# Kernel tuning notes

Hardware: AMD Instinct MI355X
Metric: run time of the kernel (lower is better)

The kernel has to match this reference:

```python
import jax, jax.numpy as jnp
import numpy as np
import math

B, T, D, H = 1, 2048, 1024, 16
DH = D // H  # 64


def relative_shift(x):
    # x: [B, H, T, S] -> Transformer-XL relative shift via zero-pad + reshape
    b, h, t, s = x.shape
    zero_pad = jnp.zeros((b, h, t, 1), dtype=x.dtype)
    x_padded = jnp.concatenate([zero_pad, x], axis=-1)       # [B,H,T,S+1]
    x_padded = x_padded.reshape(b, h, s + 1, t)              # [B,H,S+1,T]
    return x_padded[:, :, 1:].reshape(b, h, t, s)            # [B,H,T,S]


def setup_inputs() -> dict:
    key = jax.random.key(0)
    ks = jax.random.split(key, 9)
    std = 0.02
    return {
        "x": jax.random.normal(ks[0], (B, T, D), dtype=jnp.float32),
        "r_emb": jax.random.normal(ks[1], (T, D), dtype=jnp.float32),
        "Wq": jax.random.normal(ks[2], (D, D), dtype=jnp.float32) * std,
        "Wk": jax.random.normal(ks[3], (D, D), dtype=jnp.float32) * std,
        "Wv": jax.random.normal(ks[4], (D, D), dtype=jnp.float32) * std,
        "Wr": jax.random.normal(ks[5], (D, D), dtype=jnp.float32) * std,
        "Wo": jax.random.normal(ks[6], (D, D), dtype=jnp.float32) * std,
        "u": jax.random.normal(ks[7], (H, DH), dtype=jnp.float32) * std,
        "v_bias": jax.random.normal(ks[8], (H, DH), dtype=jnp.float32) * std,
    }


def reference(x, r_emb, Wq, Wk, Wv, Wr, Wo, u, v_bias):
    # mem=None path (the only shape-consistent path in the source), so S == T.
    b, t, d = x.shape
    s = t
    q = (x @ Wq).reshape(b, t, H, DH).transpose(0, 2, 1, 3)   # [B,H,T,DH]
    k = (x @ Wk).reshape(b, s, H, DH).transpose(0, 2, 1, 3)   # [B,H,S,DH]
    v = (x @ Wv).reshape(b, s, H, DH).transpose(0, 2, 1, 3)   # [B,H,S,DH]
    r = (r_emb @ Wr).reshape(r_emb.shape[0], H, DH)[-s:]       # [S,H,DH]

    AC = jnp.einsum('bhid,bhjd->bhij', q + u[None, :, None, :], k)
    BD = jnp.einsum('bhid,jhd->bhij', q + v_bias[None, :, None, :], r)
    BD = relative_shift(BD)

    attn = (AC + BD) / math.sqrt(DH)                           # [B,H,T,S]
    mask = jnp.tril(jnp.ones((t, s), dtype=bool))              # causal (S==T)
    attn = jnp.where(mask[None, None], attn, -jnp.inf)
    attn = jax.nn.softmax(attn, axis=-1)
    # dropout is identity in eval mode
    out = jnp.einsum('bhij,bhjd->bhid', attn, v)               # [B,H,T,DH]
    out = out.transpose(0, 2, 1, 3).reshape(b, t, d)           # [B,T,D]
    return out @ Wo
```

## Files before the change

### kernel.cpp

```cpp
#include <hip/hip_runtime.h>

typedef __bf16 bf16_t;
typedef __bf16 bf16x4v __attribute__((ext_vector_type(4)));
typedef __bf16 bf16x8 __attribute__((ext_vector_type(8)));
typedef float f32x4 __attribute__((ext_vector_type(4)));

constexpr int TT = 2048;
constexpr int DDIM = 1024;

constexpr size_t SZ_TD  = (size_t)2048 * 1024;
constexpr size_t OFF_QU = 0;
constexpr size_t OFF_QV = 1 * SZ_TD;
constexpr size_t OFF_KK = 2 * SZ_TD;
constexpr size_t OFF_RR = 3 * SZ_TD;
constexpr size_t OFF_VT = 4 * SZ_TD;
constexpr size_t OFF_AO = 5 * SZ_TD;
constexpr size_t OFF_XB = 6 * SZ_TD;
constexpr size_t OFF_RB = 7 * SZ_TD;
constexpr size_t OFF_WT = 8 * SZ_TD;
constexpr size_t SZ_W   = (size_t)1024 * 1024;

__device__ __forceinline__ f32x4 fzero4() {
  f32x4 z; z[0] = 0.f; z[1] = 0.f; z[2] = 0.f; z[3] = 0.f; return z;
}

__device__ __forceinline__ void gload16(const bf16_t* g, bf16_t* l) {
  __builtin_amdgcn_global_load_lds((const __attribute__((address_space(1))) void*)g,
                                   (__attribute__((address_space(3))) void*)l, 16, 0, 0);
}

__global__ __launch_bounds__(256) void convert_kernel(const float* __restrict__ x,
                                                      const float* __restrict__ r,
                                                      bf16_t* __restrict__ ws) {
  const int i = blockIdx.x * 256 + threadIdx.x;
  float4 a = ((const float4*)x)[i];
  float4 b = ((const float4*)r)[i];
  bf16x4v av, bv;
  av[0] = (bf16_t)a.x; av[1] = (bf16_t)a.y; av[2] = (bf16_t)a.z; av[3] = (bf16_t)a.w;
  bv[0] = (bf16_t)b.x; bv[1] = (bf16_t)b.y; bv[2] = (bf16_t)b.z; bv[3] = (bf16_t)b.w;
  ((bf16x4v*)(ws + OFF_XB))[i] = av;
  ((bf16x4v*)(ws + OFF_RB))[i] = bv;
}

__global__ __launch_bounds__(256) void transpose_w_kernel(const float* __restrict__ Wq,
                                                          const float* __restrict__ Wk,
                                                          const float* __restrict__ Wv,
                                                          const float* __restrict__ Wr,
                                                          const float* __restrict__ Wo,
                                                          bf16_t* __restrict__ ws) {
  const int k0 = blockIdx.x * 64, n0 = blockIdx.y * 64, wsel = blockIdx.z;
  const float* W = (wsel == 0) ? Wq : (wsel == 1) ? Wk : (wsel == 2) ? Wv : (wsel == 3) ? Wr : Wo;
  bf16_t* Wt = ws + OFF_WT + (size_t)wsel * SZ_W;
  __shared__ float tile[64][65];
  const int tid = threadIdx.x;
#pragma unroll
  for (int it = 0; it < 4; ++it) {
    int g = tid + it * 256; int rr = g >> 4; int c4 = (g & 15) * 4;
    float4 v = *(const float4*)&W[(size_t)(k0 + rr) * DDIM + n0 + c4];
    tile[rr][c4] = v.x; tile[rr][c4 + 1] = v.y; tile[rr][c4 + 2] = v.z; tile[rr][c4 + 3] = v.w;
  }
  __syncthreads();
#pragma unroll
  for (int it = 0; it < 4; ++it) {
    int g = tid + it * 256; int nr = g >> 4; int c4 = (g & 15) * 4;
    bf16x4v o;
    o[0] = (bf16_t)tile[c4 + 0][nr]; o[1] = (bf16_t)tile[c4 + 1][nr];
    o[2] = (bf16_t)tile[c4 + 2][nr]; o[3] = (bf16_t)tile[c4 + 3][nr];
    *(bf16x4v*)&Wt[(size_t)(n0 + nr) * DDIM + k0 + c4] = o;
  }
}

__device__ __forceinline__ void gemm128_core(const bf16_t* __restrict__ A,
                                             const bf16_t* __restrict__ Bt,
                                             int i0, int n0, int kbeg, int kend,
                                             f32x4 acc[4][4],
                                             bf16_t* As, bf16_t* Bs) {
  const int tid = threadIdx.x, lane = tid & 63, wv = tid >> 6;
  const int wr = (wv >> 1) * 64, wc = (wv & 1) * 64;
  const int sr = tid >> 2, scc = (tid & 3) * 8;
  const int l15 = lane & 15, lg8 = (lane >> 4) * 8;
  for (int k0 = kbeg; k0 < kend; k0 += 32) {
    __syncthreads();
    gload16(&A[(size_t)(i0 + sr) * DDIM + k0 + scc],       &As[sr * 32 + scc]);
    gload16(&A[(size_t)(i0 + 64 + sr) * DDIM + k0 + scc],  &As[(64 + sr) * 32 + scc]);
    gload16(&Bt[(size_t)(n0 + sr) * DDIM + k0 + scc],      &Bs[sr * 32 + scc]);
    gload16(&Bt[(size_t)(n0 + 64 + sr) * DDIM + k0 + scc], &Bs[(64 + sr) * 32 + scc]);
    __syncthreads();
    bf16x8 af[4], bfv[4];
#pragma unroll
    for (int m = 0; m < 4; ++m) af[m] = *(const bf16x8*)&As[(wr + m * 16 + l15) * 32 + lg8];
#pragma unroll
    for (int n = 0; n < 4; ++n) bfv[n] = *(const bf16x8*)&Bs[(wc + n * 16 + l15) * 32 + lg8];
#pragma unroll
    for (int m = 0; m < 4; ++m)
#pragma unroll
      for (int n = 0; n < 4; ++n)
        acc[m][n] = __builtin_amdgcn_mfma_f32_16x16x32_bf16(af[m], bfv[n], acc[m][n], 0, 0, 0);
  }
}

__global__ __launch_bounds__(256) void proj_kernel(const bf16_t* wsc, bf16_t* wsd,
                                                   const float* __restrict__ u,
                                                   const float* __restrict__ vb) {
  const int z = blockIdx.z;
  const int i0 = blockIdx.x * 128, n0 = blockIdx.y * 64;
  const bf16_t* A = wsc + ((z == 3) ? OFF_RB : OFF_XB);
  const bf16_t* Bt = wsc + OFF_WT + (size_t)z * SZ_W;
  __shared__ bf16_t As[128 * 32];
  __shared__ bf16_t Bs[64 * 32];
  const int tid = threadIdx.x, lane = tid & 63, wv = tid >> 6;
  const int wr = (wv >> 1) * 64, wc = (wv & 1) * 32;
  const int sr = tid >> 2, scc = (tid & 3) * 8;
  const int l15 = lane & 15, lg8 = (lane >> 4) * 8, lr4 = (lane >> 4) * 4;
  f32x4 acc[4][2];
#pragma unroll
  for (int m = 0; m < 4; ++m)
#pragma unroll
    for (int n = 0; n < 2; ++n) acc[m][n] = fzero4();

  for (int k0 = 0; k0 < DDIM; k0 += 32) {
    __syncthreads();
    gload16(&A[(size_t)(i0 + sr) * DDIM + k0 + scc],      &As[sr * 32 + scc]);
    gload16(&A[(size_t)(i0 + 64 + sr) * DDIM + k0 + scc], &As[(64 + sr) * 32 + scc]);
    gload16(&Bt[(size_t)(n0 + sr) * DDIM + k0 + scc],     &Bs[sr * 32 + scc]);
    __syncthreads();
    bf16x8 af[4], bfv[2];
#pragma unroll
    for (int m = 0; m < 4; ++m) af[m] = *(const bf16x8*)&As[(wr + m * 16 + l15) * 32 + lg8];
#pragma unroll
    for (int n = 0; n < 2; ++n) bfv[n] = *(const bf16x8*)&Bs[(wc + n * 16 + l15) * 32 + lg8];
#pragma unroll
    for (int m = 0; m < 4; ++m)
#pragma unroll
      for (int n = 0; n < 2; ++n)
        acc[m][n] = __builtin_amdgcn_mfma_f32_16x16x32_bf16(af[m], bfv[n], acc[m][n], 0, 0, 0);
  }

#pragma unroll
  for (int mm = 0; mm < 4; ++mm)
#pragma unroll
    for (int nn = 0; nn < 2; ++nn)
#pragma unroll
      for (int rg = 0; rg < 4; ++rg) {
        const int row = i0 + wr + mm * 16 + lr4 + rg;
        const int col = n0 + wc + nn * 16 + l15;
        const float val = acc[mm][nn][rg];
        const int hh = col >> 6, dh = col & 63;
        if (z == 0) {
          wsd[OFF_QU + ((size_t)hh * TT + row) * 64 + dh] = (bf16_t)(val + u[col]);
          wsd[OFF_QV + ((size_t)hh * TT + row) * 64 + dh] = (bf16_t)(val + vb[col]);
        } else if (z == 1) {
          wsd[OFF_KK + ((size_t)hh * TT + row) * 64 + dh] = (bf16_t)val;
        } else if (z == 2) {
          wsd[OFF_VT + ((size_t)hh * 64 + dh) * TT + row] = (bf16_t)val;
        } else {
          wsd[OFF_RR + ((size_t)hh * TT + (TT - 1 - row)) * 64 + dh] = (bf16_t)val;
        }
      }
}

#define SOFTPV(AC, PBX, PLX, QBASE, OO, MRUN, LRUN)                                        \
  {                                                                                        \
    float sc[4][4];                                                                        \
    float smax = -3e38f;                                                                   \
    _Pragma("unroll") for (int nt = 0; nt < 4; ++nt)                                       \
      _Pragma("unroll") for (int rg = 0; rg < 4; ++rg) {                                   \
        const int jj = nt * 16 + lg * 4 + rg;                                              \
        float v = (AC[nt][rg] + PBX[(l15 + 63 - jj) * 18 + l15]) * 0.125f;                 \
        v = (j0 + jj > (QBASE) + l15) ? -1e30f : v;                                        \
        smax = fmaxf(smax, v);                                                             \
        sc[nt][rg] = v;                                                                    \
      }                                                                                    \
    smax = fmaxf(smax, __shfl_xor(smax, 16));                                              \
    smax = fmaxf(smax, __shfl_xor(smax, 32));                                              \
    const float newm = fmaxf(MRUN, smax);                                                  \
    const float fac = __expf(MRUN - newm);                                                 \
    MRUN = newm;                                                                           \
    float pv[4][4];                                                                        \
    float rsum = 0.f;                                                                      \
    _Pragma("unroll") for (int nt = 0; nt < 4; ++nt)                                       \
      _Pragma("unroll") for (int rg = 0; rg < 4; ++rg) {                                   \
        pv[nt][rg] = __expf(sc[nt][rg] - newm);                                            \
        rsum += pv[nt][rg];                                                                \
      }                                                                                    \
    rsum += __shfl_xor(rsum, 16);                                                          \
    rsum += __shfl_xor(rsum, 32);                                                          \
    LRUN = LRUN * fac + rsum;                                                              \
    float fo[4];                                                                           \
    _Pragma("unroll") for (int rg = 0; rg < 4; ++rg) fo[rg] = __shfl(fac, lg * 4 + rg);    \
    _Pragma("unroll") for (int d = 0; d < 4; ++d)                                          \
      _Pragma("unroll") for (int rg = 0; rg < 4; ++rg) OO[d][rg] *= fo[rg];                \
    _Pragma("unroll") for (int nt = 0; nt < 4; ++nt) {                                     \
      bf16x4v pk;                                                                          \
      pk[0] = (bf16_t)pv[nt][0]; pk[1] = (bf16_t)pv[nt][1];                                \
      pk[2] = (bf16_t)pv[nt][2]; pk[3] = (bf16_t)pv[nt][3];                                \
      *(bf16x4v*)&PLX[l15 * 72 + nt * 16 + lg * 4] = pk;                                   \
    }                                                                                      \
    bf16x8 pf[2];                                                                          \
    _Pragma("unroll") for (int ks = 0; ks < 2; ++ks)                                       \
      pf[ks] = *(const bf16x8*)&PLX[l15 * 72 + ks * 32 + lg8];                             \
    _Pragma("unroll") for (int d = 0; d < 4; ++d)                                          \
      _Pragma("unroll") for (int ks = 0; ks < 2; ++ks)                                     \
        OO[d] = __builtin_amdgcn_mfma_f32_16x16x32_bf16(pf[ks], vf[d][ks], OO[d], 0, 0, 0);\
  }

__global__ __launch_bounds__(64) void attn_kernel(const bf16_t* wsc, bf16_t* wsd) {
  const int h = blockIdx.x;
  const int chunk = blockIdx.z;
  const int q32 = 63 - blockIdx.y;
  const int i0 = q32 * 32;
  const int lane = threadIdx.x & 63;
  const int l15 = lane & 15;
  const int lg = lane >> 4;
  const int lg8 = lg * 8;

  const int NT = (i0 >> 6) + 1;
  const int H = (NT + 1) >> 1;
  const int tbeg = chunk ? H : 0;
  const int tend = chunk ? NT : H;

  bf16_t* Po = wsd + ((chunk == 0) ? OFF_XB : OFF_RB) + (size_t)h * TT * 64;
  float2* ml = (float2*)(wsd + OFF_WT) + (size_t)(chunk * 16 + h) * TT;

  if (tbeg >= tend) {
#pragma unroll
    for (int m = 0; m < 2; ++m)
#pragma unroll
      for (int d = 0; d < 4; ++d)
#pragma unroll
        for (int rg = 0; rg < 4; ++rg)
          Po[(size_t)(i0 + m * 16 + lg * 4 + rg) * 64 + d * 16 + l15] = (bf16_t)0.f;
    if (lg == 0) { ml[i0 + l15] = make_float2(-3e38f, 0.f); ml[i0 + 16 + l15] = make_float2(-3e38f, 0.f); }
    return;
  }

  const bf16_t* QUp = wsc + OFF_QU + (size_t)h * TT * 64;
  const bf16_t* QVp = wsc + OFF_QV + (size_t)h * TT * 64;
  const bf16_t* Kp  = wsc + OFF_KK + (size_t)h * TT * 64;
  const bf16_t* Rp  = wsc + OFF_RR + (size_t)h * TT * 64;
  const bf16_t* Vp  = wsc + OFF_VT + (size_t)h * 64 * TT;

  __shared__ float PB1[80 * 18];
  __shared__ float PB2[80 * 18];
  __shared__ bf16_t PL1[16 * 72];
  __shared__ bf16_t PL2[16 * 72];

  bf16x8 qu1[2], qv1[2], qu2[2], qv2[2];
#pragma unroll
  for (int ks = 0; ks < 2; ++ks) {
    qu1[ks] = *(const bf16x8*)&QUp[(size_t)(i0 + l15) * 64 + ks * 32 + lg8];
    qv1[ks] = *(const bf16x8*)&QVp[(size_t)(i0 + l15) * 64 + ks * 32 + lg8];
    qu2[ks] = *(const bf16x8*)&QUp[(size_t)(i0 + 16 + l15) * 64 + ks * 32 + lg8];
    qv2[ks] = *(const bf16x8*)&QVp[(size_t)(i0 + 16 + l15) * 64 + ks * 32 + lg8];
  }

  f32x4 o1[4], o2[4];
#pragma unroll
  for (int d = 0; d < 4; ++d) { o1[d] = fzero4(); o2[d] = fzero4(); }
  float m1 = -3e38f, l1 = 0.f, m2 = -3e38f, l2 = 0.f;

  for (int t = tbeg; t < tend; ++t) {
    const int j0 = t * 64;
    bf16x8 kf[4][2], rf[6][2], vf[4][2];
#pragma unroll
    for (int nt = 0; nt < 4; ++nt)
#pragma unroll
      for (int ks = 0; ks < 2; ++ks)
        kf[nt][ks] = *(const bf16x8*)&Kp[(size_t)(j0 + nt * 16 + l15) * 64 + ks * 32 + lg8];
    const int c0 = i0 - j0 - 63;
#pragma unroll
    for (int bt = 0; bt < 6; ++bt) {
      int c = c0 + bt * 16 + l15;
      c = (c < 0) ? 0 : ((c > TT - 1) ? TT - 1 : c);
#pragma unroll
      for (int ks = 0; ks < 2; ++ks)
        rf[bt][ks] = *(const bf16x8*)&Rp[(size_t)c * 64 + ks * 32 + lg8];
    }
#pragma unroll
    for (int d = 0; d < 4; ++d)
#pragma unroll
      for (int ks = 0; ks < 2; ++ks)
        vf[d][ks] = *(const bf16x8*)&Vp[(size_t)(d * 16 + l15) * TT + j0 + ks * 32 + lg8];

    f32x4 ac1[4], ac2[4];
#pragma unroll
    for (int nt = 0; nt < 4; ++nt) { ac1[nt] = fzero4(); ac2[nt] = fzero4(); }
#pragma unroll
    for (int nt = 0; nt < 4; ++nt)
#pragma unroll
      for (int ks = 0; ks < 2; ++ks) {
        ac1[nt] = __builtin_amdgcn_mfma_f32_16x16x32_bf16(kf[nt][ks], qu1[ks], ac1[nt], 0, 0, 0);
        ac2[nt] = __builtin_amdgcn_mfma_f32_16x16x32_bf16(kf[nt][ks], qu2[ks], ac2[nt], 0, 0, 0);
      }

    f32x4 bd1[5], bd2[5];
#pragma unroll
    for (int bt = 0; bt < 5; ++bt) { bd1[bt] = fzero4(); bd2[bt] = fzero4(); }
#pragma unroll
    for (int bt = 0; bt < 5; ++bt)
#pragma unroll
      for (int ks = 0; ks < 2; ++ks) {
        bd1[bt] = __builtin_amdgcn_mfma_f32_16x16x32_bf16(rf[bt][ks], qv1[ks], bd1[bt], 0, 0, 0);
        bd2[bt] = __builtin_amdgcn_mfma_f32_16x16x32_bf16(rf[bt + 1][ks], qv2[ks], bd2[bt], 0, 0, 0);
      }
#pragma unroll
    for (int bt = 0; bt < 5; ++bt)
#pragma unroll
      for (int rg = 0; rg < 4; ++rg) {
        PB1[(bt * 16 + lg * 4 + rg) * 18 + l15] = bd1[bt][rg];
        PB2[(bt * 16 + lg * 4 + rg) * 18 + l15] = bd2[bt][rg];
      }

    SOFTPV(ac1, PB1, PL1, i0, o1, m1, l1)
    SOFTPV(ac2, PB2, PL2, i0 + 16, o2, m2, l2)
  }

#pragma unroll
  for (int d = 0; d < 4; ++d)
#pragma unroll
    for (int rg = 0; rg < 4; ++rg) {
      Po[(size_t)(i0 + lg * 4 + rg) * 64 + d * 16 + l15] = (bf16_t)o1[d][rg];
      Po[(size_t)(i0 + 16 + lg * 4 + rg) * 64 + d * 16 + l15] = (bf16_t)o2[d][rg];
    }
  if (lg == 0) { ml[i0 + l15] = make_float2(m1, l1); ml[i0 + 16 + l15] = make_float2(m2, l2); }
}

__global__ __launch_bounds__(256) void combine_kernel(const bf16_t* wsc, bf16_t* wsd) {
  const int gid = blockIdx.x * 256 + threadIdx.x;
  const int row = gid >> 3;
  const int colg = (gid & 7) * 8;
  const float2* mlp = (const float2*)(wsc + OFF_WT);
  const float2 ml0 = mlp[row];
  const float2 ml1 = mlp[16 * TT + row];
  const float M = fmaxf(ml0.x, ml1.x);
  const float e0 = __expf(ml0.x - M), e1 = __expf(ml1.x - M);
  const float inv = 1.f / (ml0.y * e0 + ml1.y * e1);
  bf16x8 o0 = *(const bf16x8*)&wsc[OFF_XB + (size_t)row * 64 + colg];
  bf16x8 o1 = *(const bf16x8*)&wsc[OFF_RB + (size_t)row * 64 + colg];
  const int hh = row >> 11, tt2 = row & 2047;
  bf16x8 r;
#pragma unroll
  for (int i = 0; i < 8; ++i)
    r[i] = (bf16_t)(((float)o0[i] * e0 + (float)o1[i] * e1) * inv);
  *(bf16x8*)&wsd[OFF_AO + (size_t)tt2 * DDIM + hh * 64 + colg] = r;
}

__global__ __launch_bounds__(256) void outproj_kernel(const bf16_t* wsc, float* __restrict__ outp) {
  const int i0 = blockIdx.x * 128, n0 = blockIdx.y * 128, kz = blockIdx.z;
  const bf16_t* A = wsc + OFF_AO;
  const bf16_t* Bt = wsc + OFF_WT + 4 * SZ_W;
  __shared__ bf16_t As[128 * 32];
  __shared__ bf16_t Bs[128 * 32];
  const int lane = threadIdx.x & 63, wv = threadIdx.x >> 6;
  const int wr = (wv >> 1) * 64, wc = (wv & 1) * 64;
  const int l15 = lane & 15, lr4 = (lane >> 4) * 4;
  f32x4 acc[4][4];
#pragma unroll
  for (int m = 0; m < 4; ++m)
#pragma unroll
    for (int n = 0; n < 4; ++n) acc[m][n] = fzero4();

  gemm128_core(A, Bt, i0, n0, kz * 256, kz * 256 + 256, acc, As, Bs);

#pragma unroll
  for (int mm = 0; mm < 4; ++mm)
#pragma unroll
    for (int nn = 0; nn < 4; ++nn)
#pragma unroll
      for (int rg = 0; rg < 4; ++rg) {
        const int row = i0 + wr + mm * 16 + lr4 + rg;
        const int col = n0 + wc + nn * 16 + l15;
        atomicAdd(&outp[(size_t)row * DDIM + col], acc[mm][nn][rg]);
      }
}

extern "C" void kernel_launch(void* const* d_in, const int* in_sizes, int n_in,
                              void* d_out, int out_size, void* d_ws, size_t ws_size,
                              hipStream_t stream) {
  (void)in_sizes; (void)n_in; (void)out_size; (void)ws_size;
  const float* x    = (const float*)d_in[0];
  const float* remb = (const float*)d_in[1];
  const float* Wq   = (const float*)d_in[2];
  const float* Wk   = (const float*)d_in[3];
  const float* Wv   = (const float*)d_in[4];
  const float* Wr   = (const float*)d_in[5];
  const float* Wo   = (const float*)d_in[6];
  const float* u    = (const float*)d_in[7];
  const float* vb   = (const float*)d_in[8];
  bf16_t* ws = (bf16_t*)d_ws;
  float* outp = (float*)d_out;

  hipMemsetAsync(outp, 0, (size_t)TT * DDIM * sizeof(float), stream);
  convert_kernel<<<dim3(2048), 256, 0, stream>>>(x, remb, ws);
  transpose_w_kernel<<<dim3(16, 16, 5), 256, 0, stream>>>(Wq, Wk, Wv, Wr, Wo, ws);
  proj_kernel<<<dim3(16, 16, 4), 256, 0, stream>>>(ws, ws, u, vb);
  attn_kernel<<<dim3(16, 64, 2), 64, 0, stream>>>(ws, ws);
  combine_kernel<<<dim3(1024), 256, 0, stream>>>(ws, ws);
  outproj_kernel<<<dim3(16, 8, 4), 256, 0, stream>>>(ws, outp);
}
```

Baseline: 229.4 us.

## Fuse Q/K/V projections sharing A tile; shrink attention LDS and add occupancy hint

The projection kernel now computes Q, K and V in one block, so each loaded x tile feeds three weight tiles instead of being reloaded by three separate blocks. The R projection runs in a second z-slice. The attention kernel reuses a single PB/PL shared buffer for both query sub-tiles, defers V fragment loads until after the score MFMAs, and adds launch_bounds(64,3) to cut register and LDS pressure. In exchange, the fused projection path has three times the accumulators, and its Q/K/V blocks do three times the work of the R blocks, so the grid is imbalanced.

```diff
diff --git a/kernel.cpp b/kernel.cpp
--- a/kernel.cpp
+++ b/kernel.cpp
@@ -70,103 +70,119 @@
   }
 }
 
-__device__ __forceinline__ void gemm128_core(const bf16_t* __restrict__ A,
-                                             const bf16_t* __restrict__ Bt,
-                                             int i0, int n0, int kbeg, int kend,
-                                             f32x4 acc[4][4],
-                                             bf16_t* As, bf16_t* Bs) {
-  const int tid = threadIdx.x, lane = tid & 63, wv = tid >> 6;
-  const int wr = (wv >> 1) * 64, wc = (wv & 1) * 64;
-  const int sr = tid >> 2, scc = (tid & 3) * 8;
-  const int l15 = lane & 15, lg8 = (lane >> 4) * 8;
-  for (int k0 = kbeg; k0 < kend; k0 += 32) {
-    __syncthreads();
-    gload16(&A[(size_t)(i0 + sr) * DDIM + k0 + scc],       &As[sr * 32 + scc]);
-    gload16(&A[(size_t)(i0 + 64 + sr) * DDIM + k0 + scc],  &As[(64 + sr) * 32 + scc]);
-    gload16(&Bt[(size_t)(n0 + sr) * DDIM + k0 + scc],      &Bs[sr * 32 + scc]);
-    gload16(&Bt[(size_t)(n0 + 64 + sr) * DDIM + k0 + scc], &Bs[(64 + sr) * 32 + scc]);
-    __syncthreads();
-    bf16x8 af[4], bfv[4];
-#pragma unroll
-    for (int m = 0; m < 4; ++m) af[m] = *(const bf16x8*)&As[(wr + m * 16 + l15) * 32 + lg8];
-#pragma unroll
-    for (int n = 0; n < 4; ++n) bfv[n] = *(const bf16x8*)&Bs[(wc + n * 16 + l15) * 32 + lg8];
-#pragma unroll
-    for (int m = 0; m < 4; ++m)
-#pragma unroll
-      for (int n = 0; n < 4; ++n)
-        acc[m][n] = __builtin_amdgcn_mfma_f32_16x16x32_bf16(af[m], bfv[n], acc[m][n], 0, 0, 0);
-  }
-}
-
 __global__ __launch_bounds__(256) void proj_kernel(const bf16_t* wsc, bf16_t* wsd,
                                                    const float* __restrict__ u,
                                                    const float* __restrict__ vb) {
-  const int z = blockIdx.z;
+  const int zr = blockIdx.z;
   const int i0 = blockIdx.x * 128, n0 = blockIdx.y * 64;
-  const bf16_t* A = wsc + ((z == 3) ? OFF_RB : OFF_XB);
-  const bf16_t* Bt = wsc + OFF_WT + (size_t)z * SZ_W;
   __shared__ bf16_t As[128 * 32];
-  __shared__ bf16_t Bs[64 * 32];
+  __shared__ bf16_t Bs[3][64 * 32];
   const int tid = threadIdx.x, lane = tid & 63, wv = tid >> 6;
   const int wr = (wv >> 1) * 64, wc = (wv & 1) * 32;
   const int sr = tid >> 2, scc = (tid & 3) * 8;
   const int l15 = lane & 15, lg8 = (lane >> 4) * 8, lr4 = (lane >> 4) * 4;
-  f32x4 acc[4][2];
-#pragma unroll
-  for (int m = 0; m < 4; ++m)
-#pragma unroll
-    for (int n = 0; n < 2; ++n) acc[m][n] = fzero4();
-
-  for (int k0 = 0; k0 < DDIM; k0 += 32) {
-    __syncthreads();
-    gload16(&A[(size_t)(i0 + sr) * DDIM + k0 + scc],      &As[sr * 32 + scc]);
-    gload16(&A[(size_t)(i0 + 64 + sr) * DDIM + k0 + scc], &As[(64 + sr) * 32 + scc]);
-    gload16(&Bt[(size_t)(n0 + sr) * DDIM + k0 + scc],     &Bs[sr * 32 + scc]);
-    __syncthreads();
-    bf16x8 af[4], bfv[2];
-#pragma unroll
-    for (int m = 0; m < 4; ++m) af[m] = *(const bf16x8*)&As[(wr + m * 16 + l15) * 32 + lg8];
-#pragma unroll
-    for (int n = 0; n < 2; ++n) bfv[n] = *(const bf16x8*)&Bs[(wc + n * 16 + l15) * 32 + lg8];
+
+  if (zr == 0) {
+    const bf16_t* A  = wsc + OFF_XB;
+    const bf16_t* Bq = wsc + OFF_WT;
+    const bf16_t* Bk = wsc + OFF_WT + 1 * SZ_W;
+    const bf16_t* Bv = wsc + OFF_WT + 2 * SZ_W;
+    f32x4 accq[4][2], acck[4][2], accv[4][2];
 #pragma unroll
     for (int m = 0; m < 4; ++m)
 #pragma unroll
-      for (int n = 0; n < 2; ++n)
-        acc[m][n] = __builtin_amdgcn_mfma_f32_16x16x32_bf16(af[m], bfv[n], acc[m][n], 0, 0, 0);
-  }
-
-#pragma unroll
-  for (int mm = 0; mm < 4; ++mm)
-#pragma unroll
-    for (int nn = 0; nn < 2; ++nn)
-#pragma unroll
-      for (int rg = 0; rg < 4; ++rg) {
-        const int row = i0 + wr + mm * 16 + lr4 + rg;
-        const int col = n0 + wc + nn * 16 + l15;
-        const float val = acc[mm][nn][rg];
-        const int hh = col >> 6, dh = col & 63;
-        if (z == 0) {
-          wsd[OFF_QU + ((size_t)hh * TT + row) * 64 + dh] = (bf16_t)(val + u[col]);
-          wsd[OFF_QV + ((size_t)hh * TT + row) * 64 + dh] = (bf16_t)(val + vb[col]);
-        } else if (z == 1) {
-          wsd[OFF_KK + ((size_t)hh * TT + row) * 64 + dh] = (bf16_t)val;
-        } else if (z == 2) {
-          wsd[OFF_VT + ((size_t)hh * 64 + dh) * TT + row] = (bf16_t)val;
-        } else {
-          wsd[OFF_RR + ((size_t)hh * TT + (TT - 1 - row)) * 64 + dh] = (bf16_t)val;
+      for (int n = 0; n < 2; ++n) { accq[m][n] = fzero4(); acck[m][n] = fzero4(); accv[m][n] = fzero4(); }
+
+    for (int k0 = 0; k0 < DDIM; k0 += 32) {
+      __syncthreads();
+      gload16(&A[(size_t)(i0 + sr) * DDIM + k0 + scc],      &As[sr * 32 + scc]);
+      gload16(&A[(size_t)(i0 + 64 + sr) * DDIM + k0 + scc], &As[(64 + sr) * 32 + scc]);
+      gload16(&Bq[(size_t)(n0 + sr) * DDIM + k0 + scc],     &Bs[0][sr * 32 + scc]);
+      gload16(&Bk[(size_t)(n0 + sr) * DDIM + k0 + scc],     &Bs[1][sr * 32 + scc]);
+      gload16(&Bv[(size_t)(n0 + sr) * DDIM + k0 + scc],     &Bs[2][sr * 32 + scc]);
+      __syncthreads();
+      bf16x8 af[4], bq[2], bk[2], bv[2];
+#pragma unroll
+      for (int m = 0; m < 4; ++m) af[m] = *(const bf16x8*)&As[(wr + m * 16 + l15) * 32 + lg8];
+#pragma unroll
+      for (int n = 0; n < 2; ++n) {
+        bq[n] = *(const bf16x8*)&Bs[0][(wc + n * 16 + l15) * 32 + lg8];
+        bk[n] = *(const bf16x8*)&Bs[1][(wc + n * 16 + l15) * 32 + lg8];
+        bv[n] = *(const bf16x8*)&Bs[2][(wc + n * 16 + l15) * 32 + lg8];
+      }
+#pragma unroll
+      for (int m = 0; m < 4; ++m)
+#pragma unroll
+        for (int n = 0; n < 2; ++n) {
+          accq[m][n] = __builtin_amdgcn_mfma_f32_16x16x32_bf16(af[m], bq[n], accq[m][n], 0, 0, 0);
+          acck[m][n] = __builtin_amdgcn_mfma_f32_16x16x32_bf16(af[m], bk[n], acck[m][n], 0, 0, 0);
+          accv[m][n] = __builtin_amdgcn_mfma_f32_16x16x32_bf16(af[m], bv[n], accv[m][n], 0, 0, 0);
         }
-      }
-}
-
-#define SOFTPV(AC, PBX, PLX, QBASE, OO, MRUN, LRUN)                                        \
+    }
+
+#pragma unroll
+    for (int mm = 0; mm < 4; ++mm)
+#pragma unroll
+      for (int nn = 0; nn < 2; ++nn)
+#pragma unroll
+        for (int rg = 0; rg < 4; ++rg) {
+          const int row = i0 + wr + mm * 16 + lr4 + rg;
+          const int col = n0 + wc + nn * 16 + l15;
+          const int hh = col >> 6, dh = col & 63;
+          wsd[OFF_QU + ((size_t)hh * TT + row) * 64 + dh] = (bf16_t)(accq[mm][nn][rg] + u[col]);
+          wsd[OFF_QV + ((size_t)hh * TT + row) * 64 + dh] = (bf16_t)(accq[mm][nn][rg] + vb[col]);
+          wsd[OFF_KK + ((size_t)hh * TT + row) * 64 + dh] = (bf16_t)acck[mm][nn][rg];
+          wsd[OFF_VT + ((size_t)hh * 64 + dh) * TT + row] = (bf16_t)accv[mm][nn][rg];
+        }
+  } else {
+    const bf16_t* A  = wsc + OFF_RB;
+    const bf16_t* Bt = wsc + OFF_WT + 3 * SZ_W;
+    f32x4 acc[4][2];
+#pragma unroll
+    for (int m = 0; m < 4; ++m)
+#pragma unroll
+      for (int n = 0; n < 2; ++n) acc[m][n] = fzero4();
+
+    for (int k0 = 0; k0 < DDIM; k0 += 32) {
+      __syncthreads();
+      gload16(&A[(size_t)(i0 + sr) * DDIM + k0 + scc],      &As[sr * 32 + scc]);
+      gload16(&A[(size_t)(i0 + 64 + sr) * DDIM + k0 + scc], &As[(64 + sr) * 32 + scc]);
+      gload16(&Bt[(size_t)(n0 + sr) * DDIM + k0 + scc],     &Bs[0][sr * 32 + scc]);
+      __syncthreads();
+      bf16x8 af[4], bfv[2];
+#pragma unroll
+      for (int m = 0; m < 4; ++m) af[m] = *(const bf16x8*)&As[(wr + m * 16 + l15) * 32 + lg8];
+#pragma unroll
+      for (int n = 0; n < 2; ++n) bfv[n] = *(const bf16x8*)&Bs[0][(wc + n * 16 + l15) * 32 + lg8];
+#pragma unroll
+      for (int m = 0; m < 4; ++m)
+#pragma unroll
+        for (int n = 0; n < 2; ++n)
+          acc[m][n] = __builtin_amdgcn_mfma_f32_16x16x32_bf16(af[m], bfv[n], acc[m][n], 0, 0, 0);
+    }
+
+#pragma unroll
+    for (int mm = 0; mm < 4; ++mm)
+#pragma unroll
+      for (int nn = 0; nn < 2; ++nn)
+#pragma unroll
+        for (int rg = 0; rg < 4; ++rg) {
+          const int row = i0 + wr + mm * 16 + lr4 + rg;
+          const int col = n0 + wc + nn * 16 + l15;
+          const int hh = col >> 6, dh = col & 63;
+          wsd[OFF_RR + ((size_t)hh * TT + (TT - 1 - row)) * 64 + dh] = (bf16_t)acc[mm][nn][rg];
+        }
+  }
+}
+
+#define SOFTPV(AC, QBASE, OO, MRUN, LRUN)                                                  \
   {                                                                                        \
     float sc[4][4];                                                                        \
     float smax = -3e38f;                                                                   \
     _Pragma("unroll") for (int nt = 0; nt < 4; ++nt)                                       \
       _Pragma("unroll") for (int rg = 0; rg < 4; ++rg) {                                   \
         const int jj = nt * 16 + lg * 4 + rg;                                              \
-        float v = (AC[nt][rg] + PBX[(l15 + 63 - jj) * 18 + l15]) * 0.125f;                 \
+        float v = (AC[nt][rg] + PB[(l15 + 63 - jj) * 18 + l15]) * 0.125f;                  \
         v = (j0 + jj > (QBASE) + l15) ? -1e30f : v;                                        \
         smax = fmaxf(smax, v);                                                             \
         sc[nt][rg] = v;                                                                    \
@@ -194,17 +210,17 @@
       bf16x4v pk;                                                                          \
       pk[0] = (bf16_t)pv[nt][0]; pk[1] = (bf16_t)pv[nt][1];                                \
       pk[2] = (bf16_t)pv[nt][2]; pk[3] = (bf16_t)pv[nt][3];                                \
-      *(bf16x4v*)&PLX[l15 * 72 + nt * 16 + lg * 4] = pk;                                   \
+      *(bf16x4v*)&PL[l15 * 72 + nt * 16 + lg * 4] = pk;                                    \
     }                                                                                      \
     bf16x8 pf[2];                                                                          \
     _Pragma("unroll") for (int ks = 0; ks < 2; ++ks)                                       \
-      pf[ks] = *(const bf16x8*)&PLX[l15 * 72 + ks * 32 + lg8];                             \
+      pf[ks] = *(const bf16x8*)&PL[l15 * 72 + ks * 32 + lg8];                              \
     _Pragma("unroll") for (int d = 0; d < 4; ++d)                                          \
       _Pragma("unroll") for (int ks = 0; ks < 2; ++ks)                                     \
         OO[d] = __builtin_amdgcn_mfma_f32_16x16x32_bf16(pf[ks], vf[d][ks], OO[d], 0, 0, 0);\
   }
 
-__global__ __launch_bounds__(64) void attn_kernel(const bf16_t* wsc, bf16_t* wsd) {
+__global__ __launch_bounds__(64, 3) void attn_kernel(const bf16_t* wsc, bf16_t* wsd) {
   const int h = blockIdx.x;
   const int chunk = blockIdx.z;
   const int q32 = 63 - blockIdx.y;
@@ -240,10 +256,8 @@
   const bf16_t* Rp  = wsc + OFF_RR + (size_t)h * TT * 64;
   const bf16_t* Vp  = wsc + OFF_VT + (size_t)h * 64 * TT;
 
-  __shared__ float PB1[80 * 18];
-  __shared__ float PB2[80 * 18];
-  __shared__ bf16_t PL1[16 * 72];
-  __shared__ bf16_t PL2[16 * 72];
+  __shared__ float PB[80 * 18];
+  __shared__ bf16_t PL[16 * 72];
 
   bf16x8 qu1[2], qv1[2], qu2[2], qv2[2];
 #pragma unroll
@@ -261,7 +275,7 @@
 
   for (int t = tbeg; t < tend; ++t) {
     const int j0 = t * 64;
-    bf16x8 kf[4][2], rf[6][2], vf[4][2];
+    bf16x8 kf[4][2], rf[6][2];
 #pragma unroll
     for (int nt = 0; nt < 4; ++nt)
 #pragma unroll
@@ -276,11 +290,6 @@
       for (int ks = 0; ks < 2; ++ks)
         rf[bt][ks] = *(const bf16x8*)&Rp[(size_t)c * 64 + ks * 32 + lg8];
     }
-#pragma unroll
-    for (int d = 0; d < 4; ++d)
-#pragma unroll
-      for (int ks = 0; ks < 2; ++ks)
-        vf[d][ks] = *(const bf16x8*)&Vp[(size_t)(d * 16 + l15) * TT + j0 + ks * 32 + lg8];
 
     f32x4 ac1[4], ac2[4];
 #pragma unroll
@@ -303,16 +312,27 @@
         bd1[bt] = __builtin_amdgcn_mfma_f32_16x16x32_bf16(rf[bt][ks], qv1[ks], bd1[bt], 0, 0, 0);
         bd2[bt] = __builtin_amdgcn_mfma_f32_16x16x32_bf16(rf[bt + 1][ks], qv2[ks], bd2[bt], 0, 0, 0);
       }
+
+    bf16x8 vf[4][2];
+#pragma unroll
+    for (int d = 0; d < 4; ++d)
+#pragma unroll
+      for (int ks = 0; ks < 2; ++ks)
+        vf[d][ks] = *(const bf16x8*)&Vp[(size_t)(d * 16 + l15) * TT + j0 + ks * 32 + lg8];
+
 #pragma unroll
     for (int bt = 0; bt < 5; ++bt)
 #pragma unroll
-      for (int rg = 0; rg < 4; ++rg) {
-        PB1[(bt * 16 + lg * 4 + rg) * 18 + l15] = bd1[bt][rg];
-        PB2[(bt * 16 + lg * 4 + rg) * 18 + l15] = bd2[bt][rg];
-      }
-
-    SOFTPV(ac1, PB1, PL1, i0, o1, m1, l1)
-    SOFTPV(ac2, PB2, PL2, i0 + 16, o2, m2, l2)
+      for (int rg = 0; rg < 4; ++rg)
+        PB[(bt * 16 + lg * 4 + rg) * 18 + l15] = bd1[bt][rg];
+    SOFTPV(ac1, i0, o1, m1, l1)
+
+#pragma unroll
+    for (int bt = 0; bt < 5; ++bt)
+#pragma unroll
+      for (int rg = 0; rg < 4; ++rg)
+        PB[(bt * 16 + lg * 4 + rg) * 18 + l15] = bd2[bt][rg];
+    SOFTPV(ac2, i0 + 16, o2, m2, l2)
   }
 
 #pragma unroll
@@ -343,6 +363,35 @@
   for (int i = 0; i < 8; ++i)
     r[i] = (bf16_t)(((float)o0[i] * e0 + (float)o1[i] * e1) * inv);
   *(bf16x8*)&wsd[OFF_AO + (size_t)tt2 * DDIM + hh * 64 + colg] = r;
+}
+
+__device__ __forceinline__ void gemm128_core(const bf16_t* __restrict__ A,
+                                             const bf16_t* __restrict__ Bt,
+                                             int i0, int n0, int kbeg, int kend,
+                                             f32x4 acc[4][4],
+                                             bf16_t* As, bf16_t* Bs) {
+  const int tid = threadIdx.x, lane = tid & 63, wv = tid >> 6;
+  const int wr = (wv >> 1) * 64, wc = (wv & 1) * 64;
+  const int sr = tid >> 2, scc = (tid & 3) * 8;
+  const int l15 = lane & 15, lg8 = (lane >> 4) * 8;
+  for (int k0 = kbeg; k0 < kend; k0 += 32) {
+    __syncthreads();
+    gload16(&A[(size_t)(i0 + sr) * DDIM + k0 + scc],       &As[sr * 32 + scc]);
+    gload16(&A[(size_t)(i0 + 64 + sr) * DDIM + k0 + scc],  &As[(64 + sr) * 32 + scc]);
+    gload16(&Bt[(size_t)(n0 + sr) * DDIM + k0 + scc],      &Bs[sr * 32 + scc]);
+    gload16(&Bt[(size_t)(n0 + 64 + sr) * DDIM + k0 + scc], &Bs[(64 + sr) * 32 + scc]);
+    __syncthreads();
+    bf16x8 af[4], bfv[4];
+#pragma unroll
+    for (int m = 0; m < 4; ++m) af[m] = *(const bf16x8*)&As[(wr + m * 16 + l15) * 32 + lg8];
+#pragma unroll
+    for (int n = 0; n < 4; ++n) bfv[n] = *(const bf16x8*)&Bs[(wc + n * 16 + l15) * 32 + lg8];
+#pragma unroll
+    for (int m = 0; m < 4; ++m)
+#pragma unroll
+      for (int n = 0; n < 4; ++n)
+        acc[m][n] = __builtin_amdgcn_mfma_f32_16x16x32_bf16(af[m], bfv[n], acc[m][n], 0, 0, 0);
+  }
 }
 
 __global__ __launch_bounds__(256) void outproj_kernel(const bf16_t* wsc, float* __restrict__ outp) {
@@ -393,7 +442,7 @@
   hipMemsetAsync(outp, 0, (size_t)TT * DDIM * sizeof(float), stream);
   convert_kernel<<<dim3(2048), 256, 0, stream>>>(x, remb, ws);
   transpose_w_kernel<<<dim3(16, 16, 5), 256, 0, stream>>>(Wq, Wk, Wv, Wr, Wo, ws);
-  proj_kernel<<<dim3(16, 16, 4), 256, 0, stream>>>(ws, ws, u, vb);
+  proj_kernel<<<dim3(16, 16, 2), 256, 0, stream>>>(ws, ws, u, vb);
   attn_kernel<<<dim3(16, 64, 2), 64, 0, stream>>>(ws, ws);
   combine_kernel<<<dim3(1024), 256, 0, stream>>>(ws, ws);
   outproj_kernel<<<dim3(16, 8, 4), 256, 0, stream>>>(ws, outp);
```

Result: slower. 280.2 us (+22.1%).
